# Kernel optimization log

Measured on AMD Instinct MI355X. Metric: run time of the kernel, lower is better.

Reference implementation:

```python
import jax, jax.numpy as jnp
import numpy as np

EPS = 1e-5
N, E, IN, H, EA, T, L = 20000, 80000, 64, 32, 32, 64, 3


def graph_norm(h, w, b, ms):
    # PyG GraphNorm over a single graph: per-feature mean/var over all nodes
    mean = jnp.mean(h, axis=0, keepdims=True)
    out = h - ms * mean
    var = jnp.mean(out * out, axis=0, keepdims=True)
    return out / jnp.sqrt(var + EPS) * w + b


def setup_inputs() -> dict:
    key = jax.random.key(0)
    ks = jax.random.split(key, 24)
    s = 0.05
    inp = {
        'x': jax.random.normal(ks[0], (N, IN), jnp.float32),
        'edge_attr': jax.random.uniform(ks[1], (E, EA), dtype=jnp.float32),
        'edge_index': jax.random.randint(ks[2], (2, E), 0, N, jnp.int32),
        # initial projection in_dim -> hidden
        'init_W': jax.random.normal(ks[3], (IN, H), jnp.float32) * s,
        'init_b': jnp.zeros((H,), jnp.float32),
        # per-layer edge MLP: edge_attr_dim -> H*H (then ReLU)
        'edge_mlp_W': jax.random.normal(ks[4], (L, EA, H * H), jnp.float32) * s,
        'edge_mlp_b': jnp.zeros((L, H * H), jnp.float32),
        # NNConv root weight and bias
        'root_W': jax.random.normal(ks[5], (L, H, H), jnp.float32) * s,
        'root_b': jnp.zeros((L, H), jnp.float32),
        # per-layer GraphNorm params
        'gn_w': jnp.ones((L, H), jnp.float32),
        'gn_b': jnp.zeros((L, H), jnp.float32),
        'gn_ms': jnp.ones((L, H), jnp.float32),
        # per-layer dense transition: 2H -> H
        'trans_W': jax.random.normal(ks[6], (L, 2 * H, H), jnp.float32) * s,
        'trans_b': jnp.zeros((L, H), jnp.float32),
        # final transition H -> T and final GraphNorm
        'final_W': jax.random.normal(ks[7], (H, T), jnp.float32) * s,
        'final_b': jnp.zeros((T,), jnp.float32),
        'fgn_w': jnp.ones((T,), jnp.float32),
        'fgn_b': jnp.zeros((T,), jnp.float32),
        'fgn_ms': jnp.ones((T,), jnp.float32),
    }
    return inp


def reference(x, edge_attr, edge_index, init_W, init_b, edge_mlp_W, edge_mlp_b,
              root_W, root_b, gn_w, gn_b, gn_ms, trans_W, trans_b,
              final_W, final_b, fgn_w, fgn_b, fgn_ms):
    src, dst = edge_index[0], edge_index[1]
    n_nodes = x.shape[0]
    h = x @ init_W + init_b  # [N, H]
    for i in range(L):
        # edge-conditioned per-edge weight matrices [E, H, H]
        ew = jax.nn.relu(edge_attr @ edge_mlp_W[i] + edge_mlp_b[i]).reshape(-1, H, H)
        # gather source node feats, per-edge matmul, scatter-add to targets
        msg = jnp.einsum('ei,eio->eo', h[src], ew)  # [E, H]
        agg = jax.ops.segment_sum(msg, dst, num_segments=n_nodes)
        conv = agg + h @ root_W[i] + root_b[i]
        # GraphNorm + ReLU + residual (in_channels == out_channels)
        hc = jax.nn.relu(graph_norm(conv, gn_w[i], gn_b[i], gn_ms[i])) + h
        # dense transition on [h, h_conv]
        h = jax.nn.relu(jnp.concatenate([h, hc], axis=1) @ trans_W[i] + trans_b[i])
    out = h @ final_W + final_b
    return jax.nn.relu(graph_norm(out, fgn_w, fgn_b, fgn_ms))
```

## Files before the change

kernel.cpp:

```cpp
#include <hip/hip_runtime.h>

namespace {

constexpr int kN  = 20000;
constexpr int kE  = 80000;
constexpr int kIn = 64;
constexpr int kH  = 32;
constexpr int kEA = 32;
constexpr int kT  = 64;
constexpr int kL  = 3;
constexpr float kEps = 1e-5f;

typedef __attribute__((ext_vector_type(8))) short bf16x8;
typedef __attribute__((ext_vector_type(4))) float f32x4;

__device__ inline unsigned short f2bf(float f) {
  unsigned u = __builtin_bit_cast(unsigned, f);
  unsigned r = (u + 0x7fff + ((u >> 16) & 1)) >> 16;
  return (unsigned short)r;
}
__device__ inline float bf2f(unsigned short s) {
  unsigned u = ((unsigned)s) << 16;
  return __builtin_bit_cast(float, u);
}

__global__ __launch_bounds__(256) void hist_dst(const int* __restrict__ ei,
                                                int* __restrict__ cnt,
                                                int* __restrict__ rank) {
  const int e = blockIdx.x * 256 + threadIdx.x;
  if (e < kE) rank[e] = atomicAdd(&cnt[ei[kE + e]], 1);
}

__global__ __launch_bounds__(1024) void scan_nodes(const int* __restrict__ cnt,
                                                   int* __restrict__ off) {
  __shared__ int wsum[16];
  __shared__ int woff[16];
  const int tid = threadIdx.x, lane = tid & 63, wid = tid >> 6;
  constexpr int CH = 20;
  const int base = tid * CH;
  int v[CH];
  int s = 0;
#pragma unroll
  for (int j = 0; j < CH; ++j) {
    const int i = base + j;
    const int c = (i < kN) ? cnt[i] : 0;
    v[j] = s;
    s += c;
  }
  int x = s;
#pragma unroll
  for (int d = 1; d < 64; d <<= 1) {
    int y = __shfl_up(x, d);
    if (lane >= d) x += y;
  }
  if (lane == 63) wsum[wid] = x;
  __syncthreads();
  if (tid < 16) {
    int t = wsum[tid];
    int xx = t;
#pragma unroll
    for (int d = 1; d < 16; d <<= 1) {
      int y = __shfl_up(xx, d);
      if (tid >= d) xx += y;
    }
    woff[tid] = xx - t;
  }
  __syncthreads();
  const int thrbase = woff[wid] + (x - s);
#pragma unroll
  for (int j = 0; j < CH; ++j) {
    const int i = base + j;
    if (i < kN) off[i] = thrbase + v[j];
  }
}

__global__ __launch_bounds__(256) void pack_w(const float* __restrict__ emW,
                                              unsigned short* __restrict__ wbf) {
  const int idx = blockIdx.x * 256 + threadIdx.x;
  if (idx >= kL * 64 * 64) return;
  const int lane = idx & 63, ct = (idx >> 6) & 63, l = idx >> 12;
  const int k0 = (lane >> 4) * 8, c = ct * 16 + (lane & 15);
  const float* W = emW + (size_t)l * kEA * kH * kH;
  unsigned out[4];
#pragma unroll
  for (int p = 0; p < 4; ++p) {
    unsigned lo = f2bf(W[(size_t)(k0 + 2 * p) * (kH * kH) + c]);
    unsigned hi = f2bf(W[(size_t)(k0 + 2 * p + 1) * (kH * kH) + c]);
    out[p] = lo | (hi << 16);
  }
  *reinterpret_cast<uint4*>(wbf + (size_t)idx * 8) =
      make_uint4(out[0], out[1], out[2], out[3]);
}

__global__ __launch_bounds__(64) void init_proj(
    const float* __restrict__ x, const float* __restrict__ W,
    const float* __restrict__ b, float* __restrict__ h) {
  __shared__ float Wl[kIn * kH];
  __shared__ float bl[kH];
  const int tid = threadIdx.x;
  {
    const float4* Ws = reinterpret_cast<const float4*>(W);
    float4* Wd = reinterpret_cast<float4*>(Wl);
    for (int j = tid; j < kIn * kH / 4; j += 64) Wd[j] = Ws[j];
  }
  if (tid < kH) bl[tid] = b[tid];
  __syncthreads();
  const int node = blockIdx.x * 64 + tid;
  if (node >= kN) return;
  float xr[kIn];
  const float4* xp = reinterpret_cast<const float4*>(x + (size_t)node * kIn);
#pragma unroll
  for (int k4 = 0; k4 < kIn / 4; ++k4) {
    float4 v = xp[k4];
    xr[k4 * 4 + 0] = v.x; xr[k4 * 4 + 1] = v.y;
    xr[k4 * 4 + 2] = v.z; xr[k4 * 4 + 3] = v.w;
  }
  float* hp = h + (size_t)node * kH;
#pragma unroll
  for (int o = 0; o < kH; ++o) {
    float acc = bl[o];
#pragma unroll
    for (int k = 0; k < kIn; ++k) acc = fmaf(xr[k], Wl[k * kH + o], acc);
    hp[o] = acc;
  }
}

constexpr int HP  = 40;
constexpr int MPW = 36;
__global__ __launch_bounds__(256) void edge_msg_mfma(
    const float* __restrict__ attr, const int* __restrict__ ei,
    const int* __restrict__ off, const int* __restrict__ rank,
    const float* __restrict__ h, const unsigned short* __restrict__ wbf,
    const float* __restrict__ bm, float* __restrict__ msg_buf) {
  __shared__ float bml[kH * kH];
  __shared__ unsigned short hbuf[4][16 * HP];
  __shared__ float mbuf[4][16 * MPW];
  const int tid = threadIdx.x;
  const int wv = tid >> 6, lane = tid & 63;
  const int lr = lane & 15, lg = lane >> 4;
  const int base = (blockIdx.x * 4 + wv) * 16;

  for (int j = tid; j < kH * kH; j += 256) bml[j] = bm[j];

  bf16x8 Af;
  {
    const float4* ap = reinterpret_cast<const float4*>(
        attr + (size_t)(base + lr) * kEA + lg * 8);
    float4 a0 = ap[0], a1 = ap[1];
    Af[0] = (short)f2bf(a0.x); Af[1] = (short)f2bf(a0.y);
    Af[2] = (short)f2bf(a0.z); Af[3] = (short)f2bf(a0.w);
    Af[4] = (short)f2bf(a1.x); Af[5] = (short)f2bf(a1.y);
    Af[6] = (short)f2bf(a1.z); Af[7] = (short)f2bf(a1.w);
  }

  {
    const int er = lane >> 2, q = lane & 3;
    const int src = ei[base + er];
    const float4* hp4 =
        reinterpret_cast<const float4*>(h + (size_t)src * kH + q * 8);
    float4 h0 = hp4[0], h1 = hp4[1];
    uint2 p0 = make_uint2(f2bf(h0.x) | ((unsigned)f2bf(h0.y) << 16),
                          f2bf(h0.z) | ((unsigned)f2bf(h0.w) << 16));
    uint2 p1 = make_uint2(f2bf(h1.x) | ((unsigned)f2bf(h1.y) << 16),
                          f2bf(h1.z) | ((unsigned)f2bf(h1.w) << 16));
    *reinterpret_cast<uint2*>(&hbuf[wv][0] + er * HP + q * 8) = p0;
    *reinterpret_cast<uint2*>(&hbuf[wv][0] + er * HP + q * 8 + 4) = p1;
  }

  __syncthreads();

  float ma[4][2] = {{0.f, 0.f}, {0.f, 0.f}, {0.f, 0.f}, {0.f, 0.f}};
  const unsigned short* hrow = &hbuf[wv][0];

#pragma unroll
  for (int g = 0; g < 4; ++g) {
    bf16x8 hv0 = *reinterpret_cast<const bf16x8*>(hrow + (lg * 4 + 0) * HP + g * 8);
    bf16x8 hv1 = *reinterpret_cast<const bf16x8*>(hrow + (lg * 4 + 1) * HP + g * 8);
    bf16x8 hv2 = *reinterpret_cast<const bf16x8*>(hrow + (lg * 4 + 2) * HP + g * 8);
    bf16x8 hv3 = *reinterpret_cast<const bf16x8*>(hrow + (lg * 4 + 3) * HP + g * 8);
#pragma unroll
    for (int i8 = 0; i8 < 8; ++i8) {
      const int il = g * 8 + i8;
      bf16x8 B0 = *reinterpret_cast<const bf16x8*>(
          wbf + ((size_t)(il * 2 + 0) * 64 + lane) * 8);
      bf16x8 B1 = *reinterpret_cast<const bf16x8*>(
          wbf + ((size_t)(il * 2 + 1) * 64 + lane) * 8);
      const float b0 = bml[il * kH + lr];
      const float b1 = bml[il * kH + 16 + lr];
      f32x4 c0, c1;
      c0[0] = b0; c0[1] = b0; c0[2] = b0; c0[3] = b0;
      c1[0] = b1; c1[1] = b1; c1[2] = b1; c1[3] = b1;
      c0 = __builtin_amdgcn_mfma_f32_16x16x32_bf16(Af, B0, c0, 0, 0, 0);
      c1 = __builtin_amdgcn_mfma_f32_16x16x32_bf16(Af, B1, c1, 0, 0, 0);
      const float h0 = bf2f((unsigned short)hv0[i8]);
      const float h1 = bf2f((unsigned short)hv1[i8]);
      const float h2 = bf2f((unsigned short)hv2[i8]);
      const float h3 = bf2f((unsigned short)hv3[i8]);
      ma[0][0] = fmaf(fmaxf(c0[0], 0.f), h0, ma[0][0]);
      ma[1][0] = fmaf(fmaxf(c0[1], 0.f), h1, ma[1][0]);
      ma[2][0] = fmaf(fmaxf(c0[2], 0.f), h2, ma[2][0]);
      ma[3][0] = fmaf(fmaxf(c0[3], 0.f), h3, ma[3][0]);
      ma[0][1] = fmaf(fmaxf(c1[0], 0.f), h0, ma[0][1]);
      ma[1][1] = fmaf(fmaxf(c1[1], 0.f), h1, ma[1][1]);
      ma[2][1] = fmaf(fmaxf(c1[2], 0.f), h2, ma[2][1]);
      ma[3][1] = fmaf(fmaxf(c1[3], 0.f), h3, ma[3][1]);
    }
  }

  float* mrow = &mbuf[wv][0];
#pragma unroll
  for (int r = 0; r < 4; ++r) {
    mrow[(lg * 4 + r) * MPW + lr] = ma[r][0];
    mrow[(lg * 4 + r) * MPW + 16 + lr] = ma[r][1];
  }
  {
    const int er = lane >> 2, q = lane & 3;
    const int e = base + er;
    const int mp = off[ei[kE + e]] + rank[e];
    float4 v0 = *reinterpret_cast<const float4*>(mrow + er * MPW + q * 8);
    float4 v1 = *reinterpret_cast<const float4*>(mrow + er * MPW + q * 8 + 4);
    float* orow = msg_buf + (size_t)mp * kH + q * 8;
    *reinterpret_cast<float4*>(orow) = v0;
    *reinterpret_cast<float4*>(orow + 4) = v1;
  }
}

__global__ __launch_bounds__(256) void agg_root_stats(
    const float* __restrict__ msg, const int* __restrict__ off,
    const int* __restrict__ cnt, const float* __restrict__ h,
    const float* __restrict__ W, const float* __restrict__ b,
    float* __restrict__ conv, float* __restrict__ stats) {
  __shared__ float Wl[kH * kH];
  __shared__ float bl[kH];
  __shared__ float buf[256 * (kH + 1)];
  const int tid = threadIdx.x;
  {
    const float4* Ws = reinterpret_cast<const float4*>(W);
    float4* Wd = reinterpret_cast<float4*>(Wl);
    if (tid < kH * kH / 4) Wd[tid] = Ws[tid];
  }
  if (tid < kH) bl[tid] = b[tid];
  __syncthreads();
  const int node = blockIdx.x * 256 + tid;
  const bool act = node < kN;
  float acc[kH];
#pragma unroll
  for (int o = 0; o < kH; ++o) acc[o] = 0.f;
  if (act) {
#pragma unroll
    for (int o = 0; o < kH; ++o) acc[o] = bl[o];
    const int s = off[node], c = cnt[node];
    for (int j = 0; j < c; ++j) {
      const float4* mp =
          reinterpret_cast<const float4*>(msg + (size_t)(s + j) * kH);
#pragma unroll
      for (int o4 = 0; o4 < kH / 4; ++o4) {
        float4 v = mp[o4];
        acc[o4 * 4 + 0] += v.x; acc[o4 * 4 + 1] += v.y;
        acc[o4 * 4 + 2] += v.z; acc[o4 * 4 + 3] += v.w;
      }
    }
    float hr[kH];
    const float4* hp = reinterpret_cast<const float4*>(h + (size_t)node * kH);
#pragma unroll
    for (int i4 = 0; i4 < kH / 4; ++i4) {
      float4 v = hp[i4];
      hr[i4 * 4 + 0] = v.x; hr[i4 * 4 + 1] = v.y;
      hr[i4 * 4 + 2] = v.z; hr[i4 * 4 + 3] = v.w;
    }
#pragma unroll
    for (int o = 0; o < kH; ++o) {
      float a = acc[o];
#pragma unroll
      for (int i = 0; i < kH; ++i) a = fmaf(hr[i], Wl[i * kH + o], a);
      acc[o] = a;
    }
    float* cp = conv + (size_t)node * kH;
#pragma unroll
    for (int o4 = 0; o4 < kH / 4; ++o4)
      *reinterpret_cast<float4*>(cp + o4 * 4) =
          make_float4(acc[o4 * 4], acc[o4 * 4 + 1], acc[o4 * 4 + 2],
                      acc[o4 * 4 + 3]);
  }
#pragma unroll
  for (int o = 0; o < kH; ++o) buf[tid * (kH + 1) + o] = act ? acc[o] : 0.f;
  __syncthreads();
  if (tid < kH) {
    float s = 0.f, q = 0.f;
#pragma unroll 8
    for (int r = 0; r < 256; ++r) {
      float v = buf[r * (kH + 1) + tid];
      s += v;
      q = fmaf(v, v, q);
    }
    atomicAdd(stats + tid, s);
    atomicAdd(stats + kH + tid, q);
  }
}

__global__ __launch_bounds__(64) void norm_trans(
    const float* __restrict__ conv, const float* __restrict__ stats,
    const float* __restrict__ gw, const float* __restrict__ gb,
    const float* __restrict__ gms, const float* __restrict__ Wt,
    const float* __restrict__ tb, float* __restrict__ h) {
  __shared__ float Wl[2 * kH * kH];
  __shared__ float tbl[kH];
  __shared__ float meanl[kH], rstdl[kH], gwl[kH], gbl[kH];
  const int tid = threadIdx.x;
  {
    const float4* Ws = reinterpret_cast<const float4*>(Wt);
    float4* Wd = reinterpret_cast<float4*>(Wl);
    for (int j = tid; j < 2 * kH * kH / 4; j += 64) Wd[j] = Ws[j];
  }
  if (tid < kH) {
    tbl[tid] = tb[tid];
    float m = stats[tid] * (1.f / kN);
    float q = stats[kH + tid] * (1.f / kN);
    float msv = gms[tid];
    float var = q - m * m * msv * (2.f - msv);
    meanl[tid] = msv * m;
    rstdl[tid] = rsqrtf(var + kEps);
    gwl[tid] = gw[tid];
    gbl[tid] = gb[tid];
  }
  __syncthreads();
  const int node = blockIdx.x * 64 + tid;
  if (node >= kN) return;
  float in_[2 * kH];
  const float* hp = h + (size_t)node * kH;
  const float* cp = conv + (size_t)node * kH;
#pragma unroll
  for (int i = 0; i < kH; ++i) in_[i] = hp[i];
#pragma unroll
  for (int o = 0; o < kH; ++o) {
    float v = cp[o];
    in_[kH + o] =
        fmaxf((v - meanl[o]) * rstdl[o] * gwl[o] + gbl[o], 0.f) + in_[o];
  }
  float* hw = h + (size_t)node * kH;
#pragma unroll
  for (int o = 0; o < kH; ++o) {
    float acc = tbl[o];
#pragma unroll
    for (int k = 0; k < 2 * kH; ++k) acc = fmaf(in_[k], Wl[k * kH + o], acc);
    hw[o] = fmaxf(acc, 0.f);
  }
}

__global__ __launch_bounds__(64) void final_lin(
    const float* __restrict__ h, const float* __restrict__ W,
    const float* __restrict__ b, float* __restrict__ out,
    float* __restrict__ stats) {
  __shared__ float Wl[kH * kT];
  __shared__ float bl[kT];
  __shared__ float buf[64 * (kT + 1)];
  const int tid = threadIdx.x;
  {
    const float4* Ws = reinterpret_cast<const float4*>(W);
    float4* Wd = reinterpret_cast<float4*>(Wl);
    for (int j = tid; j < kH * kT / 4; j += 64) Wd[j] = Ws[j];
  }
  if (tid < kT) bl[tid] = b[tid];
  __syncthreads();
  const int node = blockIdx.x * 64 + tid;
  const bool act = node < kN;
  float hr[kH];
  if (act) {
    const float4* hp = reinterpret_cast<const float4*>(h + (size_t)node * kH);
#pragma unroll
    for (int i4 = 0; i4 < kH / 4; ++i4) {
      float4 v = hp[i4];
      hr[i4 * 4 + 0] = v.x; hr[i4 * 4 + 1] = v.y;
      hr[i4 * 4 + 2] = v.z; hr[i4 * 4 + 3] = v.w;
    }
  } else {
#pragma unroll
    for (int i = 0; i < kH; ++i) hr[i] = 0.f;
  }
  float* op = out + (size_t)node * kT;
#pragma unroll
  for (int o = 0; o < kT; ++o) {
    float acc = 0.f;
    if (act) {
      acc = bl[o];
#pragma unroll
      for (int i = 0; i < kH; ++i) acc = fmaf(hr[i], Wl[i * kT + o], acc);
      op[o] = acc;
    }
    buf[tid * (kT + 1) + o] = act ? acc : 0.f;
  }
  __syncthreads();
  if (tid < kT) {
    float s = 0.f, q = 0.f;
#pragma unroll 8
    for (int r = 0; r < 64; ++r) {
      float v = buf[r * (kT + 1) + tid];
      s += v;
      q = fmaf(v, v, q);
    }
    atomicAdd(stats + tid, s);
    atomicAdd(stats + kT + tid, q);
  }
}

__global__ __launch_bounds__(64) void final_norm(
    const float* __restrict__ stats, const float* __restrict__ w,
    const float* __restrict__ b, const float* __restrict__ ms,
    float* __restrict__ out) {
  __shared__ float meanl[kT], rstdl[kT], wl2[kT], bl2[kT];
  const int tid = threadIdx.x;
  if (tid < kT) {
    float m = stats[tid] * (1.f / kN);
    float q = stats[kT + tid] * (1.f / kN);
    float msv = ms[tid];
    float var = q - m * m * msv * (2.f - msv);
    meanl[tid] = msv * m;
    rstdl[tid] = rsqrtf(var + kEps);
    wl2[tid] = w[tid];
    bl2[tid] = b[tid];
  }
  __syncthreads();
  const int node = blockIdx.x * 64 + tid;
  if (node >= kN) return;
  float* op = out + (size_t)node * kT;
#pragma unroll
  for (int o4 = 0; o4 < kT / 4; ++o4) {
    float4 v = *reinterpret_cast<const float4*>(op + o4 * 4);
    float r[4] = {v.x, v.y, v.z, v.w};
#pragma unroll
    for (int j = 0; j < 4; ++j) {
      int o = o4 * 4 + j;
      r[j] = fmaxf((r[j] - meanl[o]) * rstdl[o] * wl2[o] + bl2[o], 0.f);
    }
    *reinterpret_cast<float4*>(op + o4 * 4) =
        make_float4(r[0], r[1], r[2], r[3]);
  }
}

}

extern "C" void kernel_launch(void* const* d_in, const int* in_sizes, int n_in,
                              void* d_out, int out_size, void* d_ws,
                              size_t ws_size, hipStream_t stream) {
  const float* x     = (const float*)d_in[0];
  const float* eattr = (const float*)d_in[1];
  const int*   eidx  = (const int*)d_in[2];
  const float* initW = (const float*)d_in[3];
  const float* initb = (const float*)d_in[4];
  const float* emW   = (const float*)d_in[5];
  const float* emb   = (const float*)d_in[6];
  const float* rW    = (const float*)d_in[7];
  const float* rb    = (const float*)d_in[8];
  const float* gnw   = (const float*)d_in[9];
  const float* gnb   = (const float*)d_in[10];
  const float* gnms  = (const float*)d_in[11];
  const float* tW    = (const float*)d_in[12];
  const float* tb    = (const float*)d_in[13];
  const float* fW    = (const float*)d_in[14];
  const float* fb    = (const float*)d_in[15];
  const float* fgw   = (const float*)d_in[16];
  const float* fgb   = (const float*)d_in[17];
  const float* fgms  = (const float*)d_in[18];
  float* out = (float*)d_out;

  float* h     = (float*)d_ws;
  float* conv  = h + (size_t)kN * kH;
  float* msg   = conv + (size_t)kN * kH;
  unsigned short* wbf = (unsigned short*)(msg + (size_t)kE * kH);
  float* stats = (float*)(wbf + (size_t)kL * 64 * 64 * 8);
  int* cnt    = (int*)(stats + 512);
  int* off    = cnt + kN;
  int* rank   = off + kN;

  const int node64  = (kN + 63) / 64;
  const int node256 = (kN + 255) / 256;
  const int edgeBlocks = kE / 64;

  hipMemsetAsync(stats, 0, (512 + kN) * sizeof(float), stream);
  pack_w<<<kL * 64 * 64 / 256, 256, 0, stream>>>(emW, wbf);
  init_proj<<<node64, 64, 0, stream>>>(x, initW, initb, h);
  hist_dst<<<(kE + 255) / 256, 256, 0, stream>>>(eidx, cnt, rank);
  scan_nodes<<<1, 1024, 0, stream>>>(cnt, off);

  for (int l = 0; l < kL; ++l) {
    float* st = stats + l * 128;
    edge_msg_mfma<<<edgeBlocks, 256, 0, stream>>>(
        eattr, eidx, off, rank, h, wbf + (size_t)l * 64 * 64 * 8,
        emb + (size_t)l * kH * kH, msg);
    agg_root_stats<<<node256, 256, 0, stream>>>(
        msg, off, cnt, h, rW + (size_t)l * kH * kH, rb + l * kH, conv, st);
    norm_trans<<<node64, 64, 0, stream>>>(
        conv, st, gnw + l * kH, gnb + l * kH, gnms + l * kH,
        tW + (size_t)l * 2 * kH * kH, tb + l * kH, h);
  }
  final_lin<<<node64, 64, 0, stream>>>(h, fW, fb, out, stats + 3 * 128);
  final_norm<<<node64, 64, 0, stream>>>(stats + 3 * 128, fgw, fgb, fgms, out);
}
```

Measured before the change: 219.9 us.

## Fuse aggregation, GraphNorm and transition via grid-wide atomic barrier

Merges agg_root_stats with norm_trans, and final_lin with final_norm, into single kernels. Each pair is joined by a software grid barrier: an atomic counter per layer, spin-waited on by thread 0 of every block. The conv and final outputs stay in registers instead of round-tripping through global memory, and two launches per stage become one. The barrier is only safe if every block is co-resident (79 blocks of 256 and 313 blocks of 64 should fit on the device). Spinning adds latency and would deadlock if the blocks could not all be resident.

```diff
diff --git a/kernel.cpp b/kernel.cpp
--- a/kernel.cpp
+++ b/kernel.cpp
@@ -225,30 +225,46 @@
   }
 }
 
-__global__ __launch_bounds__(256) void agg_root_stats(
+__global__ __launch_bounds__(256) void layer_fused(
     const float* __restrict__ msg, const int* __restrict__ off,
-    const int* __restrict__ cnt, const float* __restrict__ h,
-    const float* __restrict__ W, const float* __restrict__ b,
-    float* __restrict__ conv, float* __restrict__ stats) {
-  __shared__ float Wl[kH * kH];
-  __shared__ float bl[kH];
+    const int* __restrict__ cnt, float* __restrict__ h,
+    const float* __restrict__ rW, const float* __restrict__ rb,
+    float* __restrict__ stats, int* __restrict__ done,
+    const float* __restrict__ gw, const float* __restrict__ gb,
+    const float* __restrict__ gms, const float* __restrict__ tW,
+    const float* __restrict__ tb) {
+  __shared__ float Wr[kH * kH];
+  __shared__ float Wt[2 * kH * kH];
+  __shared__ float rbl[kH], tbl[kH], gwl[kH], gbl[kH], gmsl[kH];
   __shared__ float buf[256 * (kH + 1)];
+  __shared__ float meanl[kH], rstdl[kH];
   const int tid = threadIdx.x;
   {
-    const float4* Ws = reinterpret_cast<const float4*>(W);
-    float4* Wd = reinterpret_cast<float4*>(Wl);
+    const float4* Ws = reinterpret_cast<const float4*>(rW);
+    float4* Wd = reinterpret_cast<float4*>(Wr);
     if (tid < kH * kH / 4) Wd[tid] = Ws[tid];
   }
-  if (tid < kH) bl[tid] = b[tid];
+  {
+    const float4* Ws = reinterpret_cast<const float4*>(tW);
+    float4* Wd = reinterpret_cast<float4*>(Wt);
+    for (int j = tid; j < 2 * kH * kH / 4; j += 256) Wd[j] = Ws[j];
+  }
+  if (tid < kH) {
+    rbl[tid] = rb[tid];
+    tbl[tid] = tb[tid];
+    gwl[tid] = gw[tid];
+    gbl[tid] = gb[tid];
+    gmsl[tid] = gms[tid];
+  }
   __syncthreads();
   const int node = blockIdx.x * 256 + tid;
   const bool act = node < kN;
-  float acc[kH];
-#pragma unroll
-  for (int o = 0; o < kH; ++o) acc[o] = 0.f;
+  float hr[kH], acc[kH];
+#pragma unroll
+  for (int o = 0; o < kH; ++o) { acc[o] = 0.f; hr[o] = 0.f; }
   if (act) {
 #pragma unroll
-    for (int o = 0; o < kH; ++o) acc[o] = bl[o];
+    for (int o = 0; o < kH; ++o) acc[o] = rbl[o];
     const int s = off[node], c = cnt[node];
     for (int j = 0; j < c; ++j) {
       const float4* mp =
@@ -260,7 +276,6 @@
         acc[o4 * 4 + 2] += v.z; acc[o4 * 4 + 3] += v.w;
       }
     }
-    float hr[kH];
     const float4* hp = reinterpret_cast<const float4*>(h + (size_t)node * kH);
 #pragma unroll
     for (int i4 = 0; i4 < kH / 4; ++i4) {
@@ -272,15 +287,9 @@
     for (int o = 0; o < kH; ++o) {
       float a = acc[o];
 #pragma unroll
-      for (int i = 0; i < kH; ++i) a = fmaf(hr[i], Wl[i * kH + o], a);
+      for (int i = 0; i < kH; ++i) a = fmaf(hr[i], Wr[i * kH + o], a);
       acc[o] = a;
     }
-    float* cp = conv + (size_t)node * kH;
-#pragma unroll
-    for (int o4 = 0; o4 < kH / 4; ++o4)
-      *reinterpret_cast<float4*>(cp + o4 * 4) =
-          make_float4(acc[o4 * 4], acc[o4 * 4 + 1], acc[o4 * 4 + 2],
-                      acc[o4 * 4 + 3]);
   }
 #pragma unroll
   for (int o = 0; o < kH; ++o) buf[tid * (kH + 1) + o] = act ? acc[o] : 0.f;
@@ -296,64 +305,60 @@
     atomicAdd(stats + tid, s);
     atomicAdd(stats + kH + tid, q);
   }
-}
-
-__global__ __launch_bounds__(64) void norm_trans(
-    const float* __restrict__ conv, const float* __restrict__ stats,
-    const float* __restrict__ gw, const float* __restrict__ gb,
-    const float* __restrict__ gms, const float* __restrict__ Wt,
-    const float* __restrict__ tb, float* __restrict__ h) {
-  __shared__ float Wl[2 * kH * kH];
-  __shared__ float tbl[kH];
-  __shared__ float meanl[kH], rstdl[kH], gwl[kH], gbl[kH];
-  const int tid = threadIdx.x;
-  {
-    const float4* Ws = reinterpret_cast<const float4*>(Wt);
-    float4* Wd = reinterpret_cast<float4*>(Wl);
-    for (int j = tid; j < 2 * kH * kH / 4; j += 64) Wd[j] = Ws[j];
-  }
+  __syncthreads();
+  __threadfence();
+  if (tid == 0) {
+    __hip_atomic_fetch_add(done, 1, __ATOMIC_ACQ_REL,
+                           __HIP_MEMORY_SCOPE_AGENT);
+    while (__hip_atomic_load(done, __ATOMIC_ACQUIRE,
+                             __HIP_MEMORY_SCOPE_AGENT) < (int)gridDim.x) {
+      __builtin_amdgcn_s_sleep(8);
+    }
+  }
+  __syncthreads();
   if (tid < kH) {
-    tbl[tid] = tb[tid];
-    float m = stats[tid] * (1.f / kN);
-    float q = stats[kH + tid] * (1.f / kN);
-    float msv = gms[tid];
-    float var = q - m * m * msv * (2.f - msv);
+    float s = __hip_atomic_load(&stats[tid], __ATOMIC_RELAXED,
+                                __HIP_MEMORY_SCOPE_AGENT);
+    float q = __hip_atomic_load(&stats[kH + tid], __ATOMIC_RELAXED,
+                                __HIP_MEMORY_SCOPE_AGENT);
+    float m = s * (1.f / kN);
+    float qq = q * (1.f / kN);
+    float msv = gmsl[tid];
+    float var = qq - m * m * msv * (2.f - msv);
     meanl[tid] = msv * m;
     rstdl[tid] = rsqrtf(var + kEps);
-    gwl[tid] = gw[tid];
-    gbl[tid] = gb[tid];
-  }
-  __syncthreads();
-  const int node = blockIdx.x * 64 + tid;
-  if (node >= kN) return;
-  float in_[2 * kH];
-  const float* hp = h + (size_t)node * kH;
-  const float* cp = conv + (size_t)node * kH;
-#pragma unroll
-  for (int i = 0; i < kH; ++i) in_[i] = hp[i];
-#pragma unroll
-  for (int o = 0; o < kH; ++o) {
-    float v = cp[o];
-    in_[kH + o] =
-        fmaxf((v - meanl[o]) * rstdl[o] * gwl[o] + gbl[o], 0.f) + in_[o];
-  }
-  float* hw = h + (size_t)node * kH;
-#pragma unroll
-  for (int o = 0; o < kH; ++o) {
-    float acc = tbl[o];
-#pragma unroll
-    for (int k = 0; k < 2 * kH; ++k) acc = fmaf(in_[k], Wl[k * kH + o], acc);
-    hw[o] = fmaxf(acc, 0.f);
-  }
-}
-
-__global__ __launch_bounds__(64) void final_lin(
+  }
+  __syncthreads();
+  if (act) {
+    float hc[kH];
+#pragma unroll
+    for (int o = 0; o < kH; ++o)
+      hc[o] = fmaxf((acc[o] - meanl[o]) * rstdl[o] * gwl[o] + gbl[o], 0.f) +
+              hr[o];
+    float* hw = h + (size_t)node * kH;
+#pragma unroll
+    for (int o = 0; o < kH; ++o) {
+      float a = tbl[o];
+#pragma unroll
+      for (int k = 0; k < kH; ++k) {
+        a = fmaf(hr[k], Wt[k * kH + o], a);
+        a = fmaf(hc[k], Wt[(kH + k) * kH + o], a);
+      }
+      hw[o] = fmaxf(a, 0.f);
+    }
+  }
+}
+
+__global__ __launch_bounds__(64) void final_fused(
     const float* __restrict__ h, const float* __restrict__ W,
-    const float* __restrict__ b, float* __restrict__ out,
-    float* __restrict__ stats) {
+    const float* __restrict__ b, float* __restrict__ stats,
+    int* __restrict__ done, const float* __restrict__ gw,
+    const float* __restrict__ gb, const float* __restrict__ gms,
+    float* __restrict__ out) {
   __shared__ float Wl[kH * kT];
   __shared__ float bl[kT];
   __shared__ float buf[64 * (kT + 1)];
+  __shared__ float meanl[kT], rstdl[kT], wl2[kT], bl2[kT];
   const int tid = threadIdx.x;
   {
     const float4* Ws = reinterpret_cast<const float4*>(W);
@@ -364,7 +369,9 @@
   __syncthreads();
   const int node = blockIdx.x * 64 + tid;
   const bool act = node < kN;
-  float hr[kH];
+  float hr[kH], ov[kT];
+#pragma unroll
+  for (int i = 0; i < kH; ++i) hr[i] = 0.f;
   if (act) {
     const float4* hp = reinterpret_cast<const float4*>(h + (size_t)node * kH);
 #pragma unroll
@@ -373,24 +380,17 @@
       hr[i4 * 4 + 0] = v.x; hr[i4 * 4 + 1] = v.y;
       hr[i4 * 4 + 2] = v.z; hr[i4 * 4 + 3] = v.w;
     }
-  } else {
-#pragma unroll
-    for (int i = 0; i < kH; ++i) hr[i] = 0.f;
-  }
-  float* op = out + (size_t)node * kT;
+  }
 #pragma unroll
   for (int o = 0; o < kT; ++o) {
-    float acc = 0.f;
-    if (act) {
-      acc = bl[o];
-#pragma unroll
-      for (int i = 0; i < kH; ++i) acc = fmaf(hr[i], Wl[i * kT + o], acc);
-      op[o] = acc;
-    }
-    buf[tid * (kT + 1) + o] = act ? acc : 0.f;
-  }
-  __syncthreads();
-  if (tid < kT) {
+    float a = act ? bl[o] : 0.f;
+#pragma unroll
+    for (int i = 0; i < kH; ++i) a = fmaf(hr[i], Wl[i * kT + o], a);
+    ov[o] = act ? a : 0.f;
+    buf[tid * (kT + 1) + o] = ov[o];
+  }
+  __syncthreads();
+  {
     float s = 0.f, q = 0.f;
 #pragma unroll 8
     for (int r = 0; r < 64; ++r) {
@@ -401,39 +401,45 @@
     atomicAdd(stats + tid, s);
     atomicAdd(stats + kT + tid, q);
   }
-}
-
-__global__ __launch_bounds__(64) void final_norm(
-    const float* __restrict__ stats, const float* __restrict__ w,
-    const float* __restrict__ b, const float* __restrict__ ms,
-    float* __restrict__ out) {
-  __shared__ float meanl[kT], rstdl[kT], wl2[kT], bl2[kT];
-  const int tid = threadIdx.x;
-  if (tid < kT) {
-    float m = stats[tid] * (1.f / kN);
-    float q = stats[kT + tid] * (1.f / kN);
-    float msv = ms[tid];
-    float var = q - m * m * msv * (2.f - msv);
+  __syncthreads();
+  __threadfence();
+  if (tid == 0) {
+    __hip_atomic_fetch_add(done, 1, __ATOMIC_ACQ_REL,
+                           __HIP_MEMORY_SCOPE_AGENT);
+    while (__hip_atomic_load(done, __ATOMIC_ACQUIRE,
+                             __HIP_MEMORY_SCOPE_AGENT) < (int)gridDim.x) {
+      __builtin_amdgcn_s_sleep(8);
+    }
+  }
+  __syncthreads();
+  {
+    float s = __hip_atomic_load(&stats[tid], __ATOMIC_RELAXED,
+                                __HIP_MEMORY_SCOPE_AGENT);
+    float q = __hip_atomic_load(&stats[kT + tid], __ATOMIC_RELAXED,
+                                __HIP_MEMORY_SCOPE_AGENT);
+    float m = s * (1.f / kN);
+    float qq = q * (1.f / kN);
+    float msv = gms[tid];
+    float var = qq - m * m * msv * (2.f - msv);
     meanl[tid] = msv * m;
     rstdl[tid] = rsqrtf(var + kEps);
-    wl2[tid] = w[tid];
-    bl2[tid] = b[tid];
-  }
-  __syncthreads();
-  const int node = blockIdx.x * 64 + tid;
-  if (node >= kN) return;
-  float* op = out + (size_t)node * kT;
-#pragma unroll
-  for (int o4 = 0; o4 < kT / 4; ++o4) {
-    float4 v = *reinterpret_cast<const float4*>(op + o4 * 4);
-    float r[4] = {v.x, v.y, v.z, v.w};
-#pragma unroll
-    for (int j = 0; j < 4; ++j) {
-      int o = o4 * 4 + j;
-      r[j] = fmaxf((r[j] - meanl[o]) * rstdl[o] * wl2[o] + bl2[o], 0.f);
-    }
-    *reinterpret_cast<float4*>(op + o4 * 4) =
-        make_float4(r[0], r[1], r[2], r[3]);
+    wl2[tid] = gw[tid];
+    bl2[tid] = gb[tid];
+  }
+  __syncthreads();
+  if (act) {
+    float* op = out + (size_t)node * kT;
+#pragma unroll
+    for (int o4 = 0; o4 < kT / 4; ++o4) {
+      float r[4];
+#pragma unroll
+      for (int j = 0; j < 4; ++j) {
+        const int o = o4 * 4 + j;
+        r[j] = fmaxf((ov[o] - meanl[o]) * rstdl[o] * wl2[o] + bl2[o], 0.f);
+      }
+      *reinterpret_cast<float4*>(op + o4 * 4) =
+          make_float4(r[0], r[1], r[2], r[3]);
+    }
   }
 }
 
@@ -464,11 +470,11 @@
   float* out = (float*)d_out;
 
   float* h     = (float*)d_ws;
-  float* conv  = h + (size_t)kN * kH;
-  float* msg   = conv + (size_t)kN * kH;
+  float* msg   = h + (size_t)kN * kH;
   unsigned short* wbf = (unsigned short*)(msg + (size_t)kE * kH);
   float* stats = (float*)(wbf + (size_t)kL * 64 * 64 * 8);
-  int* cnt    = (int*)(stats + 512);
+  int* done   = (int*)(stats + 512);
+  int* cnt    = done + 16;
   int* off    = cnt + kN;
   int* rank   = off + kN;
 
@@ -476,23 +482,21 @@
   const int node256 = (kN + 255) / 256;
   const int edgeBlocks = kE / 64;
 
-  hipMemsetAsync(stats, 0, (512 + kN) * sizeof(float), stream);
+  hipMemsetAsync(stats, 0, (512 + 16 + kN) * sizeof(float), stream);
   pack_w<<<kL * 64 * 64 / 256, 256, 0, stream>>>(emW, wbf);
   init_proj<<<node64, 64, 0, stream>>>(x, initW, initb, h);
   hist_dst<<<(kE + 255) / 256, 256, 0, stream>>>(eidx, cnt, rank);
   scan_nodes<<<1, 1024, 0, stream>>>(cnt, off);
 
   for (int l = 0; l < kL; ++l) {
-    float* st = stats + l * 128;
     edge_msg_mfma<<<edgeBlocks, 256, 0, stream>>>(
         eattr, eidx, off, rank, h, wbf + (size_t)l * 64 * 64 * 8,
         emb + (size_t)l * kH * kH, msg);
-    agg_root_stats<<<node256, 256, 0, stream>>>(
-        msg, off, cnt, h, rW + (size_t)l * kH * kH, rb + l * kH, conv, st);
-    norm_trans<<<node64, 64, 0, stream>>>(
-        conv, st, gnw + l * kH, gnb + l * kH, gnms + l * kH,
-        tW + (size_t)l * 2 * kH * kH, tb + l * kH, h);
-  }
-  final_lin<<<node64, 64, 0, stream>>>(h, fW, fb, out, stats + 3 * 128);
-  final_norm<<<node64, 64, 0, stream>>>(stats + 3 * 128, fgw, fgb, fgms, out);
-}
+    layer_fused<<<node256, 256, 0, stream>>>(
+        msg, off, cnt, h, rW + (size_t)l * kH * kH, rb + l * kH,
+        stats + l * 128, done + l, gnw + l * kH, gnb + l * kH, gnms + l * kH,
+        tW + (size_t)l * 2 * kH * kH, tb + l * kH);
+  }
+  final_fused<<<node64, 64, 0, stream>>>(h, fW, fb, stats + 3 * 128, done + 3,
+                                         fgw, fgb, fgms, out);
+}
```

After: 255.6 us. 1.16x slower.
